# Optimization experiments

Hardware: AMD Instinct MI355X
Metric: run time of the kernel (lower is better)

The kernel has to match this reference:

```python
import jax, jax.numpy as jnp
import numpy as np

B, H, W = 256, 192, 384
NF = (H // 8) * (W // 8)  # 1152 per-feature MLPs


def conv_same(x, w, b):
    # Conv2d padding='same', kernel 5, NCHW / OIHW
    y = jax.lax.conv_general_dilated(x, w, (1, 1), 'SAME',
                                     dimension_numbers=('NCHW', 'OIHW', 'NCHW'))
    return y + b[None, :, None, None]


def maxpool2(x):
    return jax.lax.reduce_window(x, -jnp.inf, jax.lax.max,
                                 (1, 1, 2, 2), (1, 1, 2, 2), 'VALID')


def setup_inputs() -> dict:
    key = jax.random.key(0)
    ks = jax.random.split(key, 16)
    s = 0.05
    return {
        'x': jax.random.normal(ks[0], (B, 1, H, W), jnp.float32),
        'mask': jax.random.uniform(ks[1], (H, W), jnp.float32),
        'c1_w': jax.random.normal(ks[2], (8, 1, 5, 5), jnp.float32) * s,
        'c1_b': jax.random.normal(ks[3], (8,), jnp.float32) * s,
        'c2_w': jax.random.normal(ks[4], (8, 8, 5, 5), jnp.float32) * s,
        'c2_b': jax.random.normal(ks[5], (8,), jnp.float32) * s,
        'c3_w': jax.random.normal(ks[6], (8, 8, 5, 5), jnp.float32) * s,
        'c3_b': jax.random.normal(ks[7], (8,), jnp.float32) * s,
        'c4_w': jax.random.normal(ks[8], (8, 8, 5, 5), jnp.float32) * s,
        'c4_b': jax.random.normal(ks[9], (8,), jnp.float32) * s,
        'W1': jax.random.normal(ks[10], (NF, 8, 32), jnp.float32) * 0.3,
        'b1': jax.random.normal(ks[11], (NF, 32), jnp.float32) * 0.05,
        'W2': jax.random.normal(ks[12], (NF, 32, 32), jnp.float32) * 0.15,
        'b2': jax.random.normal(ks[13], (NF, 32), jnp.float32) * 0.05,
        'W3': jax.random.normal(ks[14], (NF, 32), jnp.float32) * 0.15,
        'add_bias': jnp.zeros((1,), jnp.float32),
    }


def reference(x, mask, c1_w, c1_b, c2_w, c2_b, c3_w, c3_b, c4_w, c4_b,
              W1, b1, W2, b2, W3, add_bias):
    b, _, h, w = x.shape
    # 1. bilinear downsample by 0.5, align_corners=False == exact 2x2 avg pool
    xd = x.reshape(b, 1, h // 2, 2, w // 2, 2).mean(axis=(3, 5))
    # 2. conv stack (dropout p=0.7 is identity in eval)
    z = conv_same(xd, c1_w, c1_b)
    z = jax.nn.relu(conv_same(z, c2_w, c2_b))
    z = maxpool2(z)
    z = conv_same(z, c3_w, c3_b)
    z = jax.nn.relu(conv_same(z, c4_w, c4_b))
    z = maxpool2(z)                      # [B, 8, H/8, W/8]
    # 3. unroll 2D -> 1D
    hfeat = z.reshape(b, 8, -1)          # [B, 8, F]
    # 4. all per-feature MLPs as batched GEMMs (dropout p=0.2 identity in eval)
    t = jax.nn.relu(jnp.einsum('bcf,fch->bfh', hfeat, W1) + b1[None])
    t = jax.nn.relu(jnp.einsum('bfh,fhg->bfg', t, W2) + b2[None])
    feat = jnp.einsum('bfg,fg->bf', t, W3)  # [B, F]
    # 5/6. mask land regions: nearest-downscale mask by 1/8 then threshold
    m = (mask[::8, ::8] > 0.5).astype(feat.dtype).reshape(-1)
    out = jnp.sum(feat * m[None, :], axis=-1) + add_bias[0]
    return jax.nn.sigmoid(out)           # [B]
```

## Files before the change

kernel.cpp:

```cpp
#include <hip/hip_runtime.h>
#include <math.h>

typedef unsigned short ushort;
typedef unsigned int uint;
typedef __attribute__((ext_vector_type(8))) short bf16x8;
typedef __attribute__((ext_vector_type(8))) ushort ushort8;
typedef __attribute__((ext_vector_type(4))) float f32x4;

#define WT1_OFF   0
#define MV_OFF    256
#define BIAS_OFF  1536
#define BFH_OFF   1600
#define BFL_OFF   6976
#define BFP_OFF   12352
#define BUFA_OFF  16384
#define PLANE_U   9437184
#define BUFB_OFF  (BUFA_OFF + PLANE_U)
#define PART2_OFF (BUFB_OFF + PLANE_U)

__device__ __forceinline__ ushort f2bf(float f) {
    union { float f; uint u; } a; a.f = f;
    uint u = a.u;
    return (ushort)((u + 0x7FFFu + ((u >> 16) & 1u)) >> 16);
}
__device__ __forceinline__ float bf2f(ushort s) {
    union { uint u; float f; } a; a.u = ((uint)s) << 16; return a.f;
}
__device__ __forceinline__ void split_bf(float v, ushort& h, ushort& l) {
    h = f2bf(v);
    l = f2bf(v - bf2f(h));
}

__global__ void prep_kernel(const float* __restrict__ c1w, const float* __restrict__ c2w,
                            const float* __restrict__ c3w, const float* __restrict__ c4w,
                            const float* __restrict__ c2b, const float* __restrict__ c3b,
                            const float* __restrict__ c4b,
                            const float* __restrict__ mask, float* __restrict__ ws) {
    int idx = blockIdx.x * blockDim.x + threadIdx.x;
    if (idx < 200) {
        int co = idx & 7, rest = idx >> 3;
        int dx = rest % 5, dy = rest / 5;
        ws[WT1_OFF + idx] = c1w[co * 25 + dy * 5 + dx];
    }
    if (idx < 1152) {
        int i = idx / 48, j = idx % 48;
        ws[MV_OFF + idx] = (mask[i * 8 * 384 + j * 8] > 0.5f) ? 1.0f : 0.0f;
    }
    if (idx < 48) {
        int c = idx >> 4, co = idx & 15;
        const float* b = (c == 0) ? c2b : (c == 1) ? c3b : c4b;
        ws[BIAS_OFF + idx] = (co < 8) ? b[co] : 0.f;
    }
    if (idx < 1344) {
        int c = idx / 448, rem = idx % 448;
        int g = rem >> 6, l = rem & 63;
        int tg = l >> 4, co16 = l & 15;
        int tap = g * 4 + tg;
        const float* wsrc = (c == 0) ? c2w : (c == 1) ? c3w : c4w;
        ushort* bh = (ushort*)(ws + BFH_OFF) + (size_t)idx * 8;
        ushort* bl = (ushort*)(ws + BFL_OFF) + (size_t)idx * 8;
#pragma unroll
        for (int j = 0; j < 8; ++j) {
            float v = 0.f;
            if (tap < 25 && co16 < 8)
                v = wsrc[((co16 * 8 + j) * 5 + tap / 5) * 5 + (tap % 5)];
            ushort h, lo; split_bf(v, h, lo);
            bh[j] = h; bl[j] = lo;
        }
    }
    if (idx < 896) {
        int c = idx / 448 + 1, rem = idx % 448;
        int g = rem >> 6, l = rem & 63;
        int tg = l >> 4, co16 = l & 15;
        int co = co16 & 7;
        int tap = g * 4 + tg;
        const float* wsrc = (c == 1) ? c3w : c4w;
        ushort* dst = (ushort*)(ws + BFP_OFF) + (size_t)idx * 8;
#pragma unroll
        for (int j = 0; j < 8; ++j) {
            float v = 0.f;
            if (tap < 25)
                v = wsrc[((co * 8 + j) * 5 + tap / 5) * 5 + (tap % 5)];
            ushort h, lo; split_bf(v, h, lo);
            dst[j] = (co16 < 8) ? h : lo;
        }
    }
    if (idx < 48 * 256)
        ws[PART2_OFF + idx] = 0.f;
}

__global__ __launch_bounds__(512) void k1_fused(
        const float* __restrict__ x, const float* __restrict__ wt1,
        const float* __restrict__ c1b,
        const ushort* __restrict__ bfh, const ushort* __restrict__ bfl,
        const float* __restrict__ biaspad, ushort* __restrict__ z2) {
    __shared__ __align__(16) char smem0[8192];
    __shared__ ushort z1h[20 * 68 * 8];
    __shared__ ushort z1l[20 * 68 * 8];
    float (*xdbuf)[72] = reinterpret_cast<float(*)[72]>(smem0);
    ushort* z2bh = (ushort*)smem0;
    ushort* z2bl = (ushort*)(smem0 + 4096);
    const int rt = blockIdx.x, ct = blockIdx.y, b = blockIdx.z;
    const int tid = threadIdx.x;
    const int ry0 = rt * 16, cx0 = ct * 64;

    for (int i = tid; i < 24 * 36; i += 512) {
        int pr = i / 36, pj = i % 36;
        int gy = ry0 - 4 + pr, gx = cx0 - 4 + 2 * pj;
        float v0 = 0.f, v1 = 0.f;
        if (gy >= 0 && gy < 96 && gx >= 0 && gx < 192) {
            const float* p = x + (size_t)b * (192 * 384) + (2 * gy) * 384 + 2 * gx;
            float4 a = *(const float4*)p;
            float4 c = *(const float4*)(p + 384);
            v0 = (a.x + a.y + c.x + c.y) * 0.25f;
            v1 = (a.z + a.w + c.z + c.w) * 0.25f;
        }
        xdbuf[pr][2 * pj]     = v0;
        xdbuf[pr][2 * pj + 1] = v1;
    }
    __syncthreads();

    for (int i = tid; i < 20 * 68; i += 512) {
        int iy = i / 68, ix = i % 68;
        int gy = ry0 - 2 + iy, gx = cx0 - 2 + ix;
        float acc[8];
        if (gy >= 0 && gy < 96 && gx >= 0 && gx < 192) {
#pragma unroll
            for (int co = 0; co < 8; ++co) acc[co] = c1b[co];
#pragma unroll
            for (int dy = 0; dy < 5; ++dy)
#pragma unroll
                for (int dx = 0; dx < 5; ++dx) {
                    float v = xdbuf[iy + dy][ix + dx];
#pragma unroll
                    for (int co = 0; co < 8; ++co)
                        acc[co] = fmaf(v, wt1[(dy * 5 + dx) * 8 + co], acc[co]);
                }
        } else {
#pragma unroll
            for (int co = 0; co < 8; ++co) acc[co] = 0.f;
        }
        ushort8 uh, ul;
#pragma unroll
        for (int co = 0; co < 8; ++co) {
            ushort h, lo; split_bf(acc[co], h, lo);
            uh[co] = h; ul[co] = lo;
        }
        *(ushort8*)&z1h[i * 8] = uh;
        *(ushort8*)&z1l[i * 8] = ul;
    }
    __syncthreads();

    const int lane = tid & 63, w = tid >> 6;
    const int p = lane & 15, tg = lane >> 4;
    bf16x8 bwh[7], bwl[7];
#pragma unroll
    for (int g = 0; g < 7; ++g) {
        bwh[g] = *(const bf16x8*)(bfh + (size_t)(g * 64 + lane) * 8);
        bwl[g] = *(const bf16x8*)(bfl + (size_t)(g * 64 + lane) * 8);
    }
    const float bias = biaspad[lane & 15];
    int off[7];
#pragma unroll
    for (int g = 0; g < 7; ++g) {
        int t = g * 4 + tg; t = (t > 24) ? 24 : t;
        off[g] = ((t / 5) * 68 + (t % 5)) * 8;
    }
    float stash[4][2];
#pragma unroll
    for (int rl = 0; rl < 2; ++rl) {
        const int r = 2 * w + rl;
#pragma unroll
        for (int cg = 0; cg < 4; ++cg) {
            f32x4 acc = {0.f, 0.f, 0.f, 0.f};
            const int base = (r * 68 + cg * 16 + p) * 8;
#pragma unroll
            for (int g = 0; g < 7; ++g) {
                bf16x8 ah = *(const bf16x8*)&z1h[base + off[g]];
                bf16x8 al = *(const bf16x8*)&z1l[base + off[g]];
                acc = __builtin_amdgcn_mfma_f32_16x16x32_bf16(ah, bwh[g], acc, 0, 0, 0);
                acc = __builtin_amdgcn_mfma_f32_16x16x32_bf16(ah, bwl[g], acc, 0, 0, 0);
                acc = __builtin_amdgcn_mfma_f32_16x16x32_bf16(al, bwh[g], acc, 0, 0, 0);
            }
            float p0 = fmaxf(fmaxf(acc[0], acc[1]) + bias, 0.f);
            float p1 = fmaxf(fmaxf(acc[2], acc[3]) + bias, 0.f);
            if (rl == 0) {
                stash[cg][0] = p0; stash[cg][1] = p1;
            } else {
                p0 = fmaxf(p0, stash[cg][0]);
                p1 = fmaxf(p1, stash[cg][1]);
                if ((lane & 15) < 8) {
                    int pr = w;
                    int pc = cg * 8 + tg * 2;
                    ushort h0, l0, h1, l1;
                    split_bf(p0, h0, l0); split_bf(p1, h1, l1);
                    z2bh[(pr * 32 + pc) * 8 + (lane & 15)]     = h0;
                    z2bl[(pr * 32 + pc) * 8 + (lane & 15)]     = l0;
                    z2bh[(pr * 32 + pc + 1) * 8 + (lane & 15)] = h1;
                    z2bl[(pr * 32 + pc + 1) * 8 + (lane & 15)] = l1;
                }
            }
        }
    }
    __syncthreads();
    if (tid < 256) {
        int prr = tid >> 5, pcc = tid & 31;
        size_t gidx = ((size_t)(b * 48 + rt * 8 + prr) * 96 + ct * 32 + pcc) * 8;
        *(ushort8*)(z2 + gidx)           = *(const ushort8*)&z2bh[(prr * 32 + pcc) * 8];
        *(ushort8*)(z2 + PLANE_U + gidx) = *(const ushort8*)&z2bl[(prr * 32 + pcc) * 8];
    }
}

__global__ __launch_bounds__(512) void conv_mfma(
        const ushort* __restrict__ in, ushort* __restrict__ out,
        const ushort* __restrict__ bfrag, const float* __restrict__ biaspad,
        int do_relu) {
    __shared__ ushort inh[20 * 36 * 8];
    __shared__ ushort inl[20 * 36 * 8];
    __shared__ ushort outh[16 * 32 * 8];
    __shared__ ushort outl[16 * 32 * 8];
    const int rt = blockIdx.x, ctile = blockIdx.y, b = blockIdx.z;
    const int ry0 = rt * 16, cx0 = ctile * 32;
    const int tid = threadIdx.x;

    for (int u = tid; u < 20 * 36; u += 512) {
        int r = u / 36, col = u % 36;
        int gy = ry0 - 2 + r, gc = cx0 - 2 + col;
        ushort8 vh = {0, 0, 0, 0, 0, 0, 0, 0};
        ushort8 vl = vh;
        if (gy >= 0 && gy < 48 && gc >= 0 && gc < 96) {
            size_t gidx = ((size_t)(b * 48 + gy) * 96 + gc) * 8;
            vh = *(const ushort8*)(in + gidx);
            vl = *(const ushort8*)(in + PLANE_U + gidx);
        }
        *(ushort8*)&inh[u * 8] = vh;
        *(ushort8*)&inl[u * 8] = vl;
    }
    __syncthreads();

    const int lane = tid & 63, w = tid >> 6;
    const int p = lane & 15, tg = lane >> 4;
    bf16x8 bw[7];
#pragma unroll
    for (int g = 0; g < 7; ++g)
        bw[g] = *(const bf16x8*)(bfrag + (size_t)(g * 64 + lane) * 8);
    const float bias = biaspad[lane & 15];
    int off[7];
#pragma unroll
    for (int g = 0; g < 7; ++g) {
        int t = g * 4 + tg; t = (t > 24) ? 24 : t;
        off[g] = ((t / 5) * 36 + (t % 5)) * 8;
    }
#pragma unroll
    for (int rl = 0; rl < 2; ++rl) {
        const int r = 2 * w + rl;
#pragma unroll
        for (int cg = 0; cg < 2; ++cg) {
            f32x4 a1 = {0.f, 0.f, 0.f, 0.f};
            f32x4 a2 = {0.f, 0.f, 0.f, 0.f};
            const int base = (r * 36 + cg * 16 + p) * 8;
#pragma unroll
            for (int g = 0; g < 7; ++g) {
                bf16x8 ah = *(const bf16x8*)&inh[base + off[g]];
                bf16x8 al = *(const bf16x8*)&inl[base + off[g]];
                a1 = __builtin_amdgcn_mfma_f32_16x16x32_bf16(ah, bw[g], a1, 0, 0, 0);
                a2 = __builtin_amdgcn_mfma_f32_16x16x32_bf16(al, bw[g], a2, 0, 0, 0);
            }
            f32x4 s = a1 + a2;
            float tot[4];
#pragma unroll
            for (int i = 0; i < 4; ++i)
                tot[i] = s[i] + __shfl_xor(s[i], 8);
            if ((lane & 15) < 8) {
#pragma unroll
                for (int i = 0; i < 4; ++i) {
                    float v = tot[i] + bias;
                    if (do_relu) v = fmaxf(v, 0.f);
                    int px = r * 32 + cg * 16 + tg * 4 + i;
                    ushort h, lo; split_bf(v, h, lo);
                    outh[px * 8 + (lane & 15)] = h;
                    outl[px * 8 + (lane & 15)] = lo;
                }
            }
        }
    }
    __syncthreads();
    {
        int u = tid;
        int row = u / 32, col = u % 32;
        size_t gidx = ((size_t)(b * 48 + ry0 + row) * 96 + cx0 + col) * 8;
        *(ushort8*)(out + gidx)           = *(const ushort8*)&outh[u * 8];
        *(ushort8*)(out + PLANE_U + gidx) = *(const ushort8*)&outl[u * 8];
    }
}

__global__ __launch_bounds__(256) void mlp_kernel(
        const ushort* __restrict__ z4, const float* __restrict__ W1,
        const float* __restrict__ b1, const float* __restrict__ W2,
        const float* __restrict__ b2, const float* __restrict__ W3,
        const float* __restrict__ mv, float* __restrict__ part2) {
    const int f = blockIdx.x;
    const int bb = threadIdx.x;
    if (mv[f] == 0.f) return;
    const int y = f / 48, xcol = f % 48;
    size_t s0i = (((size_t)bb * 48 + 2 * y) * 96 + 2 * xcol) * 8;
    ushort8 ah0 = *(const ushort8*)(z4 + s0i);
    ushort8 ah1 = *(const ushort8*)(z4 + s0i + 8);
    ushort8 ch0 = *(const ushort8*)(z4 + s0i + 96 * 8);
    ushort8 ch1 = *(const ushort8*)(z4 + s0i + 96 * 8 + 8);
    ushort8 al0 = *(const ushort8*)(z4 + PLANE_U + s0i);
    ushort8 al1 = *(const ushort8*)(z4 + PLANE_U + s0i + 8);
    ushort8 cl0 = *(const ushort8*)(z4 + PLANE_U + s0i + 96 * 8);
    ushort8 cl1 = *(const ushort8*)(z4 + PLANE_U + s0i + 96 * 8 + 8);
    float h[8];
#pragma unroll
    for (int c = 0; c < 8; ++c) {
        float v00 = bf2f(ah0[c]) + bf2f(al0[c]);
        float v01 = bf2f(ah1[c]) + bf2f(al1[c]);
        float v10 = bf2f(ch0[c]) + bf2f(cl0[c]);
        float v11 = bf2f(ch1[c]) + bf2f(cl1[c]);
        h[c] = fmaxf(fmaxf(v00, v01), fmaxf(v10, v11));
    }

    const float* w1p = W1 + (size_t)f * 8 * 32;
    const float* b1p = b1 + (size_t)f * 32;
    float t1[32];
#pragma unroll
    for (int j = 0; j < 32; ++j) t1[j] = b1p[j];
    for (int c = 0; c < 8; ++c) {
        float hv = h[c];
        const float* wp = w1p + c * 32;
#pragma unroll
        for (int j = 0; j < 32; ++j) t1[j] = fmaf(hv, wp[j], t1[j]);
    }
#pragma unroll
    for (int j = 0; j < 32; ++j) t1[j] = fmaxf(t1[j], 0.f);

    const float* w2p = W2 + (size_t)f * 32 * 32;
    const float* b2p = b2 + (size_t)f * 32;
    float t2[32];
#pragma unroll
    for (int g = 0; g < 32; ++g) t2[g] = b2p[g];
    for (int j = 0; j < 32; ++j) {
        float tv = t1[j];
        const float* wp = w2p + j * 32;
#pragma unroll
        for (int g = 0; g < 32; ++g) t2[g] = fmaf(tv, wp[g], t2[g]);
    }
    const float* w3p = W3 + (size_t)f * 32;
    float s = 0.f;
#pragma unroll
    for (int g = 0; g < 32; ++g) s = fmaf(fmaxf(t2[g], 0.f), w3p[g], s);
    atomicAdd(&part2[(size_t)(f / 24) * 256 + bb], s);
}

__global__ void reduce2_kernel(const float* __restrict__ part2, const float* __restrict__ ab,
                               float* __restrict__ out) {
    int bb = threadIdx.x;
    float s = 0.f;
    for (int k = 0; k < 48; ++k) s += part2[(size_t)k * 256 + bb];
    s += ab[0];
    out[bb] = 1.f / (1.f + expf(-s));
}

extern "C" void kernel_launch(void* const* d_in, const int* in_sizes, int n_in,
                              void* d_out, int out_size, void* d_ws, size_t ws_size,
                              hipStream_t stream) {
    const float* x    = (const float*)d_in[0];
    const float* mask = (const float*)d_in[1];
    const float* c1w  = (const float*)d_in[2];
    const float* c1b  = (const float*)d_in[3];
    const float* c2w  = (const float*)d_in[4];
    const float* c2b  = (const float*)d_in[5];
    const float* c3w  = (const float*)d_in[6];
    const float* c3b  = (const float*)d_in[7];
    const float* c4w  = (const float*)d_in[8];
    const float* c4b  = (const float*)d_in[9];
    const float* W1   = (const float*)d_in[10];
    const float* b1   = (const float*)d_in[11];
    const float* W2   = (const float*)d_in[12];
    const float* b2   = (const float*)d_in[13];
    const float* W3   = (const float*)d_in[14];
    const float* ab   = (const float*)d_in[15];
    float* ws = (float*)d_ws;

    float*  wt1   = ws + WT1_OFF;
    float*  mv    = ws + MV_OFF;
    float*  biasp = ws + BIAS_OFF;
    ushort* bfh   = (ushort*)(ws + BFH_OFF);
    ushort* bfl   = (ushort*)(ws + BFL_OFF);
    ushort* bfp   = (ushort*)(ws + BFP_OFF);
    ushort* bufA  = (ushort*)(ws + BUFA_OFF);
    ushort* bufB  = (ushort*)(ws + BUFB_OFF);
    float*  part2 = ws + PART2_OFF;

    prep_kernel<<<48, 256, 0, stream>>>(c1w, c2w, c3w, c4w, c2b, c3b, c4b, mask, ws);
    k1_fused<<<dim3(6, 3, 256), 512, 0, stream>>>(x, wt1, c1b, bfh, bfl, biasp, bufA);
    conv_mfma<<<dim3(3, 3, 256), 512, 0, stream>>>(bufA, bufB, bfp,
                                                   biasp + 16, 0);
    conv_mfma<<<dim3(3, 3, 256), 512, 0, stream>>>(bufB, bufA, bfp + 448 * 8,
                                                   biasp + 32, 1);
    mlp_kernel<<<1152, 256, 0, stream>>>(bufA, W1, b1, W2, b2, W3, mv, part2);
    reduce2_kernel<<<1, 256, 0, stream>>>(part2, ab, (float*)d_out);
}
```

Before: 194.3 us.

## Fuse conv3 and conv4 into one kernel with halo recompute in LDS

Merges the two conv_mfma launches into a single kernel that loads a 24x40 halo tile, computes conv3 on an extended 20x36 region into LDS, then computes conv4 from LDS. This removes the global round trip of the intermediate activation planes and one kernel launch. The split-bf16 scheme changes from packed hi/lo weight fragments with a shuffle reduction to three MFMAs per tap (hh, hl, lh), which drops the separate packed-weight prep. The cost is recomputing conv3 on the halo, a larger LDS footprint, and more MFMAs per output pixel.

```diff
diff --git a/kernel.cpp b/kernel.cpp
--- a/kernel.cpp
+++ b/kernel.cpp
@@ -12,7 +12,6 @@
 #define BIAS_OFF  1536
 #define BFH_OFF   1600
 #define BFL_OFF   6976
-#define BFP_OFF   12352
 #define BUFA_OFF  16384
 #define PLANE_U   9437184
 #define BUFB_OFF  (BUFA_OFF + PLANE_U)
@@ -66,23 +65,6 @@
                 v = wsrc[((co16 * 8 + j) * 5 + tap / 5) * 5 + (tap % 5)];
             ushort h, lo; split_bf(v, h, lo);
             bh[j] = h; bl[j] = lo;
-        }
-    }
-    if (idx < 896) {
-        int c = idx / 448 + 1, rem = idx % 448;
-        int g = rem >> 6, l = rem & 63;
-        int tg = l >> 4, co16 = l & 15;
-        int co = co16 & 7;
-        int tap = g * 4 + tg;
-        const float* wsrc = (c == 1) ? c3w : c4w;
-        ushort* dst = (ushort*)(ws + BFP_OFF) + (size_t)idx * 8;
-#pragma unroll
-        for (int j = 0; j < 8; ++j) {
-            float v = 0.f;
-            if (tap < 25)
-                v = wsrc[((co * 8 + j) * 5 + tap / 5) * 5 + (tap % 5)];
-            ushort h, lo; split_bf(v, h, lo);
-            dst[j] = (co16 < 8) ? h : lo;
         }
     }
     if (idx < 48 * 256)
@@ -211,21 +193,26 @@
     }
 }
 
-__global__ __launch_bounds__(512) void conv_mfma(
+__global__ __launch_bounds__(512) void conv34_fused(
         const ushort* __restrict__ in, ushort* __restrict__ out,
-        const ushort* __restrict__ bfrag, const float* __restrict__ biaspad,
-        int do_relu) {
-    __shared__ ushort inh[20 * 36 * 8];
-    __shared__ ushort inl[20 * 36 * 8];
-    __shared__ ushort outh[16 * 32 * 8];
-    __shared__ ushort outl[16 * 32 * 8];
+        const ushort* __restrict__ bfh3, const ushort* __restrict__ bfl3,
+        const ushort* __restrict__ bfh4, const ushort* __restrict__ bfl4,
+        const float* __restrict__ biaspad3, const float* __restrict__ biaspad4) {
+    __shared__ ushort inh[24 * 40 * 8];
+    __shared__ ushort inl[24 * 40 * 8];
+    __shared__ ushort midh[20 * 36 * 8];
+    __shared__ ushort midl[20 * 36 * 8];
+    ushort* outh = inh;
+    ushort* outl = inl;
     const int rt = blockIdx.x, ctile = blockIdx.y, b = blockIdx.z;
     const int ry0 = rt * 16, cx0 = ctile * 32;
     const int tid = threadIdx.x;
-
-    for (int u = tid; u < 20 * 36; u += 512) {
-        int r = u / 36, col = u % 36;
-        int gy = ry0 - 2 + r, gc = cx0 - 2 + col;
+    const int lane = tid & 63, w = tid >> 6;
+    const int p = lane & 15, tg = lane >> 4;
+
+    for (int u = tid; u < 24 * 40; u += 512) {
+        int r = u / 40, col = u % 40;
+        int gy = ry0 - 4 + r, gc = cx0 - 4 + col;
         ushort8 vh = {0, 0, 0, 0, 0, 0, 0, 0};
         ushort8 vl = vh;
         if (gy >= 0 && gy < 48 && gc >= 0 && gc < 96) {
@@ -238,48 +225,85 @@
     }
     __syncthreads();
 
-    const int lane = tid & 63, w = tid >> 6;
-    const int p = lane & 15, tg = lane >> 4;
-    bf16x8 bw[7];
-#pragma unroll
-    for (int g = 0; g < 7; ++g)
-        bw[g] = *(const bf16x8*)(bfrag + (size_t)(g * 64 + lane) * 8);
-    const float bias = biaspad[lane & 15];
-    int off[7];
-#pragma unroll
-    for (int g = 0; g < 7; ++g) {
-        int t = g * 4 + tg; t = (t > 24) ? 24 : t;
-        off[g] = ((t / 5) * 36 + (t % 5)) * 8;
-    }
-#pragma unroll
-    for (int rl = 0; rl < 2; ++rl) {
-        const int r = 2 * w + rl;
-#pragma unroll
-        for (int cg = 0; cg < 2; ++cg) {
-            f32x4 a1 = {0.f, 0.f, 0.f, 0.f};
-            f32x4 a2 = {0.f, 0.f, 0.f, 0.f};
-            const int base = (r * 36 + cg * 16 + p) * 8;
+    {
+        bf16x8 bwh[7], bwl[7];
+#pragma unroll
+        for (int g = 0; g < 7; ++g) {
+            bwh[g] = *(const bf16x8*)(bfh3 + (size_t)(g * 64 + lane) * 8);
+            bwl[g] = *(const bf16x8*)(bfl3 + (size_t)(g * 64 + lane) * 8);
+        }
+        const float bias = biaspad3[lane & 15];
+        int off[7];
+#pragma unroll
+        for (int g = 0; g < 7; ++g) {
+            int t = g * 4 + tg; t = (t > 24) ? 24 : t;
+            off[g] = ((t / 5) * 40 + (t % 5)) * 8;
+        }
+        for (int grp = w; grp < 45; grp += 8) {
+            int pix = grp * 16 + p;
+            int r = pix / 36, c = pix % 36;
+            const int base = (r * 40 + c) * 8;
+            f32x4 acc = {0.f, 0.f, 0.f, 0.f};
 #pragma unroll
             for (int g = 0; g < 7; ++g) {
                 bf16x8 ah = *(const bf16x8*)&inh[base + off[g]];
                 bf16x8 al = *(const bf16x8*)&inl[base + off[g]];
-                a1 = __builtin_amdgcn_mfma_f32_16x16x32_bf16(ah, bw[g], a1, 0, 0, 0);
-                a2 = __builtin_amdgcn_mfma_f32_16x16x32_bf16(al, bw[g], a2, 0, 0, 0);
-            }
-            f32x4 s = a1 + a2;
-            float tot[4];
-#pragma unroll
-            for (int i = 0; i < 4; ++i)
-                tot[i] = s[i] + __shfl_xor(s[i], 8);
+                acc = __builtin_amdgcn_mfma_f32_16x16x32_bf16(ah, bwh[g], acc, 0, 0, 0);
+                acc = __builtin_amdgcn_mfma_f32_16x16x32_bf16(ah, bwl[g], acc, 0, 0, 0);
+                acc = __builtin_amdgcn_mfma_f32_16x16x32_bf16(al, bwh[g], acc, 0, 0, 0);
+            }
             if ((lane & 15) < 8) {
 #pragma unroll
                 for (int i = 0; i < 4; ++i) {
-                    float v = tot[i] + bias;
-                    if (do_relu) v = fmaxf(v, 0.f);
-                    int px = r * 32 + cg * 16 + tg * 4 + i;
+                    int pix2 = grp * 16 + tg * 4 + i;
+                    int row2 = pix2 / 36, col2 = pix2 % 36;
+                    int gy = ry0 - 2 + row2, gx = cx0 - 2 + col2;
+                    bool ok = (gy >= 0 && gy < 48 && gx >= 0 && gx < 96);
+                    float v = ok ? (acc[i] + bias) : 0.f;
                     ushort h, lo; split_bf(v, h, lo);
-                    outh[px * 8 + (lane & 15)] = h;
-                    outl[px * 8 + (lane & 15)] = lo;
+                    midh[pix2 * 8 + (lane & 15)] = h;
+                    midl[pix2 * 8 + (lane & 15)] = lo;
+                }
+            }
+        }
+    }
+    __syncthreads();
+
+    {
+        bf16x8 bwh[7], bwl[7];
+#pragma unroll
+        for (int g = 0; g < 7; ++g) {
+            bwh[g] = *(const bf16x8*)(bfh4 + (size_t)(g * 64 + lane) * 8);
+            bwl[g] = *(const bf16x8*)(bfl4 + (size_t)(g * 64 + lane) * 8);
+        }
+        const float bias = biaspad4[lane & 15];
+        int off[7];
+#pragma unroll
+        for (int g = 0; g < 7; ++g) {
+            int t = g * 4 + tg; t = (t > 24) ? 24 : t;
+            off[g] = ((t / 5) * 36 + (t % 5)) * 8;
+        }
+        for (int grp = w; grp < 32; grp += 8) {
+            int pix = grp * 16 + p;
+            int r = pix >> 5, c = pix & 31;
+            const int base = (r * 36 + c) * 8;
+            f32x4 acc = {0.f, 0.f, 0.f, 0.f};
+#pragma unroll
+            for (int g = 0; g < 7; ++g) {
+                bf16x8 ah = *(const bf16x8*)&midh[base + off[g]];
+                bf16x8 al = *(const bf16x8*)&midl[base + off[g]];
+                acc = __builtin_amdgcn_mfma_f32_16x16x32_bf16(ah, bwh[g], acc, 0, 0, 0);
+                acc = __builtin_amdgcn_mfma_f32_16x16x32_bf16(ah, bwl[g], acc, 0, 0, 0);
+                acc = __builtin_amdgcn_mfma_f32_16x16x32_bf16(al, bwh[g], acc, 0, 0, 0);
+            }
+            if ((lane & 15) < 8) {
+#pragma unroll
+                for (int i = 0; i < 4; ++i) {
+                    int pix2 = grp * 16 + tg * 4 + i;
+                    float v = fmaxf(acc[i] + bias, 0.f);
+                    ushort h, lo; split_bf(v, h, lo);
+                    outh[pix2 * 8 + (lane & 15)] = h;
+                    outl[pix2 * 8 + (lane & 15)] = lo;
                 }
             }
         }
@@ -287,7 +311,7 @@
     __syncthreads();
     {
         int u = tid;
-        int row = u / 32, col = u % 32;
+        int row = u >> 5, col = u & 31;
         size_t gidx = ((size_t)(b * 48 + ry0 + row) * 96 + cx0 + col) * 8;
         *(ushort8*)(out + gidx)           = *(const ushort8*)&outh[u * 8];
         *(ushort8*)(out + PLANE_U + gidx) = *(const ushort8*)&outl[u * 8];
@@ -389,17 +413,17 @@
     float*  biasp = ws + BIAS_OFF;
     ushort* bfh   = (ushort*)(ws + BFH_OFF);
     ushort* bfl   = (ushort*)(ws + BFL_OFF);
-    ushort* bfp   = (ushort*)(ws + BFP_OFF);
     ushort* bufA  = (ushort*)(ws + BUFA_OFF);
     ushort* bufB  = (ushort*)(ws + BUFB_OFF);
     float*  part2 = ws + PART2_OFF;
 
     prep_kernel<<<48, 256, 0, stream>>>(c1w, c2w, c3w, c4w, c2b, c3b, c4b, mask, ws);
     k1_fused<<<dim3(6, 3, 256), 512, 0, stream>>>(x, wt1, c1b, bfh, bfl, biasp, bufA);
-    conv_mfma<<<dim3(3, 3, 256), 512, 0, stream>>>(bufA, bufB, bfp,
-                                                   biasp + 16, 0);
-    conv_mfma<<<dim3(3, 3, 256), 512, 0, stream>>>(bufB, bufA, bfp + 448 * 8,
-                                                   biasp + 32, 1);
-    mlp_kernel<<<1152, 256, 0, stream>>>(bufA, W1, b1, W2, b2, W3, mv, part2);
+    conv34_fused<<<dim3(3, 3, 256), 512, 0, stream>>>(
+        bufA, bufB,
+        bfh + 448 * 8, bfl + 448 * 8,
+        bfh + 2 * 448 * 8, bfl + 2 * 448 * 8,
+        biasp + 16, biasp + 32);
+    mlp_kernel<<<1152, 256, 0, stream>>>(bufB, W1, b1, W2, b2, W3, mv, part2);
     reduce2_kernel<<<1, 256, 0, stream>>>(part2, ab, (float*)d_out);
 }
```

After: 200.9 us. 1.03x slower.
